# Kernel tuning notes

Measured on AMD Instinct MI355X. Metric: run time of the kernel, lower is better.

## Reference

```python
import jax, jax.numpy as jnp
import numpy as np

EPS = 1e-5  # torch BatchNorm default eps, eval mode with running stats

def _bn(x, g, b, m, v):
    shp = (1, -1) + (1,) * (x.ndim - 2)
    return (x - m.reshape(shp)) * (g.reshape(shp) / jnp.sqrt(v.reshape(shp) + EPS)) + b.reshape(shp)

def _lrelu(x):
    return jnp.where(x > 0, x, 0.2 * x)

def setup_inputs() -> dict:
    key = jax.random.key(0)
    ks = jax.random.split(key, 20)
    B, N, K = 4, 2048, 32
    Cin, Cf, Co = 6, 64, 64  # in_channels, feat_channels, out_channels(==nhiddens)
    f32 = jnp.float32
    def randn(k, shape, s=1.0):
        return jax.random.normal(k, shape, f32) * s
    def bnp(k, c):
        k1, k2, k3, k4 = jax.random.split(k, 4)
        return (randn(k1, (c,)), randn(k2, (c,)), randn(k3, (c,), 0.1),
                jax.random.uniform(k4, (c,), f32, 0.5, 1.5))
    inp = {
        "x": randn(ks[0], (B, Cin, N, K)),          # knn_points
        "y": randn(ks[1], (B, Cf, N, K)),           # knn_feat
        "points": randn(ks[2], (B, Cin // 2, N)),
        "feat": randn(ks[3], (B, Cf // 2, N)),
        "Wq": randn(ks[4], (Cf, Cf // 2), 0.1),
        "Wpos1": randn(ks[5], (Cin, Cin // 2), 0.1),
        "Wpos2": randn(ks[6], (Cf, Cin), 0.1),
        "Wattn": randn(ks[7], (Co * Cin, Cf), 0.1),
        "Wlin": randn(ks[8], (Co, Co), 0.1),
        "Wres": randn(ks[9], (Co, Cf), 0.1),
    }
    for name, k, c in [("q", ks[10], Cf), ("p", ks[11], Cin), ("a", ks[12], Co * Cin),
                       ("1", ks[13], Co), ("l", ks[14], Co), ("r", ks[15], Co)]:
        g, b, m, v = bnp(k, c)
        inp["g" + name], inp["b" + name], inp["m" + name], inp["v" + name] = g, b, m, v
    return inp

def reference(x, y, points, feat, Wq, Wpos1, Wpos2, Wattn, Wlin, Wres,
              gq, bq, mq, vq, gp, bp, mp, vp, ga, ba, ma, va,
              g1, b1, m1, v1, gl, bl, ml, vl, gr, br, mr, vr):
    B, Cin, N, K = x.shape
    Cf = y.shape[1]
    Co = Wattn.shape[0] // Cin
    # query projection (conv1d 1x1 == per-point GEMM) + BN + LeakyReLU
    x_q = _lrelu(_bn(jnp.einsum('oi,bin->bon', Wq, feat), gq, bq, mq, vq))   # [B,Cf,N]
    # positional branch
    pos = _lrelu(_bn(jnp.einsum('oi,bin->bon', Wpos1, points), gp, bp, mp, vp))  # [B,Cin,N]
    pos = pos[:, :, :, None] - x                                             # [B,Cin,N,K]
    pos = jnp.einsum('oi,bink->bonk', Wpos2, pos)                            # [B,Cf,N,K]
    # vector (subtraction) attention, softmax over neighbors k
    attn = x_q[:, :, :, None] - y + pos                                      # [B,Cf,N,K]
    attn = jax.nn.softmax(attn / float(np.sqrt(Cf)), axis=-1)
    attn = _bn(jnp.einsum('oi,bink->bonk', Wattn, attn), ga, ba, ma, va)     # [B,Co*Cin,N,K]
    # per-point tiny matmul: [Co,Cin] @ [Cin] for every (b,n,k)
    attn = attn.transpose(0, 2, 3, 1).reshape(B, N, K, Co, Cin)
    out = jnp.einsum('bnkoi,bnki->bonk', attn, x.transpose(0, 2, 3, 1))      # [B,Co,N,K]
    h = _lrelu(_bn(out, g1, b1, m1, v1))
    h = _bn(jnp.einsum('oi,bink->bonk', Wlin, h), gl, bl, ml, vl)
    res = _bn(jnp.einsum('oi,bink->bonk', Wres, y), gr, br, mr, vr)
    return _lrelu(h + res)
```

## Files before the change

kernel.cpp:

```cpp
#include <hip/hip_runtime.h>

constexpr int NB  = 4;
constexpr int NPT = 2048;
constexpr int KNN = 32;
constexpr int CIN = 6;
constexpr int CF  = 64;
constexpr int CO  = 64;
constexpr float EPS = 1e-5f;

typedef short bf16x8 __attribute__((ext_vector_type(8)));
typedef float f32x4  __attribute__((ext_vector_type(4)));

constexpr size_t WS_WA  = 0;
constexpr size_t WS_WL  = 49152;
constexpr size_t WS_WR  = 57344;
constexpr size_t WS_BA  = 65536;
constexpr size_t WS_BNF = 67072;

__device__ __host__ inline unsigned short bf16_rne(float f) {
  unsigned u = __builtin_bit_cast(unsigned, f);
  u += 0x7fffu + ((u >> 16) & 1u);
  return (unsigned short)(u >> 16);
}

__global__ void setup_kernel(const float *Wattn, const float *Wlin, const float *Wres,
                             const float *ga, const float *ba, const float *ma, const float *va,
                             const float *g1, const float *b1, const float *m1, const float *v1,
                             const float *gl, const float *bl, const float *ml, const float *vl,
                             const float *gr, const float *br, const float *mr, const float *vr,
                             unsigned short *WAf, unsigned short *WLf, unsigned short *WRf,
                             float *baP, float *bnf) {
  const int t = blockIdx.x * blockDim.x + threadIdx.x;
  const int stride = gridDim.x * blockDim.x;
  for (int e = t; e < 6 * 4 * 2 * 64 * 8; e += stride) {
    const int j = e & 7, l = (e >> 3) & 63, ks = (e >> 9) & 1, ot = (e >> 10) & 3, i = e >> 12;
    const int m = l & 15, cg = l >> 4;
    const int cc = ks * 32 + cg * 8 + j;
    const int row = (ot * 16 + m) * CIN + i;
    const float sa = ga[row] * rsqrtf(va[row] + EPS);
    WAf[e] = bf16_rne(Wattn[row * CF + cc] * sa);
  }
  for (int e = t; e < 4 * 2 * 64 * 8; e += stride) {
    const int j = e & 7, l = (e >> 3) & 63, ks = (e >> 9) & 1, ot = e >> 10;
    const int m = l & 15;
    const int cc = ks * 32 + (l >> 4) * 8 + j;
    const int row = ot * 16 + m;
    const float sl = gl[row] * rsqrtf(vl[row] + EPS);
    const float sr = gr[row] * rsqrtf(vr[row] + EPS);
    WLf[e] = bf16_rne(Wlin[row * CF + cc] * sl);
    WRf[e] = bf16_rne(Wres[row * CF + cc] * sr);
  }
  for (int e = t; e < 384; e += stride) {
    const int i = e >> 6, o = e & 63;
    const int j0 = o * CIN + i;
    const float sa = ga[j0] * rsqrtf(va[j0] + EPS);
    baP[e] = ba[j0] - ma[j0] * sa;
  }
  for (int e = t; e < 64; e += stride) {
    const float s1v = g1[e] * rsqrtf(v1[e] + EPS);
    bnf[e]      = s1v;
    bnf[64 + e] = b1[e] - m1[e] * s1v;
    const float slv = gl[e] * rsqrtf(vl[e] + EPS);
    const float srv = gr[e] * rsqrtf(vr[e] + EPS);
    bnf[128 + e] = (bl[e] - ml[e] * slv) + (br[e] - mr[e] * srv);
  }
}

struct Params {
  const float *x, *y, *points, *feat;
  const float *Wq, *Wpos1, *Wpos2;
  const float *gq, *bq, *mq, *vq;
  const float *gp, *bp, *mp, *vp;
  const unsigned short *WAf, *WLf, *WRf;
  const float *baP, *bnf;
  float *out;
};

__global__ __launch_bounds__(256) void fused_pt_attn(Params p) {
  const int tid  = threadIdx.x;
  const int lane = tid & 63;
  const int wid  = tid >> 6;
  const int bid  = ((blockIdx.x & 7) << 8) + (blockIdx.x >> 3);
  const int pidx = bid * 4 + wid;
  const int b    = pidx >> 11;
  const int n    = pidx & (NPT - 1);

  __shared__ unsigned short s_B[4][2048];
  __shared__ float s_d[4][192];
  __shared__ float s_f[4][32];
  unsigned short *BB = s_B[wid];
  float *dW = s_d[wid];
  float *fW = s_f[wid];

  float ftv = 0.f, ptv = 0.f;
  if (lane < 32) ftv = p.feat[((size_t)b * 32 + lane) * NPT + n];
  if (lane < 3)  ptv = p.points[((size_t)b * 3 + lane) * NPT + n];
  const int xi = lane >> 3, xk = (lane & 7) * 4;
  float4 x4 = make_float4(0.f, 0.f, 0.f, 0.f);
  if (lane < 48)
    x4 = *(const float4 *)(p.x + (((size_t)b * CIN + xi) * NPT + n) * KNN + xk);
  const float *w2p = p.Wpos2 + lane * 6;
  const float2 w2a = *(const float2 *)(w2p);
  const float2 w2b = *(const float2 *)(w2p + 2);
  const float2 w2c = *(const float2 *)(w2p + 4);
  const float w2[6] = {w2a.x, w2a.y, w2b.x, w2b.y, w2c.x, w2c.y};

  if (lane < 32) fW[lane] = ftv;

  const float pt0 = __shfl(ptv, 0), pt1 = __shfl(ptv, 1), pt2 = __shfl(ptv, 2);
  float pos1[6];
#pragma unroll
  for (int i = 0; i < 6; ++i) {
    const float a = p.Wpos1[i * 3 + 0] * pt0 + p.Wpos1[i * 3 + 1] * pt1 +
                    p.Wpos1[i * 3 + 2] * pt2;
    const float s = p.gp[i] * rsqrtf(p.vp[i] + EPS);
    const float v = fmaf(a, s, p.bp[i] - p.mp[i] * s);
    pos1[i] = v > 0.f ? v : 0.2f * v;
  }

  if (lane < 48) {
    float pi = pos1[0];
    pi = (xi == 1) ? pos1[1] : pi;
    pi = (xi == 2) ? pos1[2] : pi;
    pi = (xi == 3) ? pos1[3] : pi;
    pi = (xi == 4) ? pos1[4] : pi;
    pi = (xi == 5) ? pos1[5] : pi;
    *(float4 *)(dW + xi * 32 + xk) =
        make_float4(pi - x4.x, pi - x4.y, pi - x4.z, pi - x4.w);
  }

  float xq;
  {
    float acc = 0.f;
    const float *wq = p.Wq + lane * 32;
#pragma unroll
    for (int q = 0; q < 8; ++q) {
      const float4 w4 = *(const float4 *)(wq + q * 4);
      const float4 f4 = *(const float4 *)(fW + q * 4);
      acc = fmaf(w4.x, f4.x, fmaf(w4.y, f4.y, fmaf(w4.z, f4.z, fmaf(w4.w, f4.w, acc))));
    }
    const float s = p.gq[lane] * rsqrtf(p.vq[lane] + EPS);
    const float v = fmaf(acc, s, p.bq[lane] - p.mq[lane] * s);
    xq = v > 0.f ? v : 0.2f * v;
  }

  float pre[32];
#pragma unroll
  for (int k = 0; k < 32; ++k) pre[k] = 0.f;
#pragma unroll
  for (int i = 0; i < 6; ++i) {
    const float wv = w2[i];
#pragma unroll
    for (int q = 0; q < 8; ++q) {
      const float4 d4 = *(const float4 *)(dW + i * 32 + q * 4);
      pre[q * 4 + 0] = fmaf(wv, d4.x, pre[q * 4 + 0]);
      pre[q * 4 + 1] = fmaf(wv, d4.y, pre[q * 4 + 1]);
      pre[q * 4 + 2] = fmaf(wv, d4.z, pre[q * 4 + 2]);
      pre[q * 4 + 3] = fmaf(wv, d4.w, pre[q * 4 + 3]);
    }
  }

  const float *yrow = p.y + (((size_t)b * CF + lane) * NPT + n) * KNN;
#pragma unroll
  for (int q = 0; q < 8; ++q) {
    const float4 y4 = *(const float4 *)(yrow + q * 4);
    const float yv[4] = {y4.x, y4.y, y4.z, y4.w};
#pragma unroll
    for (int j = 0; j < 4; ++j) {
      const int k = q * 4 + j;
      BB[k * 64 + (lane ^ ((k & 7) << 3))] = bf16_rne(yv[j]);
      pre[k] = (xq - yv[j] + pre[k]) * 0.125f;
    }
  }

  const int og = lane >> 4, kl = lane & 15;
  const int swz = (kl & 7) << 3;

  bf16x8 By[2][2];
#pragma unroll
  for (int ks = 0; ks < 2; ++ks)
#pragma unroll
    for (int nt = 0; nt < 2; ++nt)
      By[ks][nt] = *(const bf16x8 *)(BB + (kl + nt * 16) * 64 +
                                     ((ks * 32 + og * 8) ^ swz));

  float mx = pre[0];
#pragma unroll
  for (int k = 1; k < 32; ++k) mx = fmaxf(mx, pre[k]);
  float sum = 0.f;
#pragma unroll
  for (int k = 0; k < 32; ++k) {
    pre[k] = __expf(pre[k] - mx);
    BB[k * 64 + (lane ^ ((k & 7) << 3))] = bf16_rne(pre[k]);
    sum += pre[k];
  }
  const float inv = 1.f / sum;

  float xvv[6][2];
#pragma unroll
  for (int i = 0; i < 6; ++i)
#pragma unroll
    for (int nt = 0; nt < 2; ++nt)
      xvv[i][nt] = pos1[i] - dW[i * 32 + kl + nt * 16];

  bf16x8 Ba[2][2];
#pragma unroll
  for (int ks = 0; ks < 2; ++ks)
#pragma unroll
    for (int nt = 0; nt < 2; ++nt)
      Ba[ks][nt] = *(const bf16x8 *)(BB + (kl + nt * 16) * 64 +
                                     ((ks * 32 + og * 8) ^ swz));

  const bf16x8 *WAv = (const bf16x8 *)p.WAf;
#pragma unroll
  for (int ot = 0; ot < 4; ++ot) {
    float out1[2][4] = {{0.f, 0.f, 0.f, 0.f}, {0.f, 0.f, 0.f, 0.f}};
#pragma unroll
    for (int i = 0; i < 6; ++i) {
      const bf16x8 A0 = WAv[((i * 4 + ot) * 2 + 0) * 64 + lane];
      const bf16x8 A1 = WAv[((i * 4 + ot) * 2 + 1) * 64 + lane];
      const f32x4 ba4 = *(const f32x4 *)(p.baP + i * 64 + ot * 16 + og * 4);
#pragma unroll
      for (int nt = 0; nt < 2; ++nt) {
        f32x4 g = {0.f, 0.f, 0.f, 0.f};
        g = __builtin_amdgcn_mfma_f32_16x16x32_bf16(A0, Ba[0][nt], g, 0, 0, 0);
        g = __builtin_amdgcn_mfma_f32_16x16x32_bf16(A1, Ba[1][nt], g, 0, 0, 0);
        const float xv = xvv[i][nt];
#pragma unroll
        for (int r = 0; r < 4; ++r)
          out1[nt][r] = fmaf(fmaf(g[r], inv, ba4[r]), xv, out1[nt][r]);
      }
    }
    const f32x4 s14 = *(const f32x4 *)(p.bnf + 0 * 64 + ot * 16 + og * 4);
    const f32x4 b14 = *(const f32x4 *)(p.bnf + 1 * 64 + ot * 16 + og * 4);
#pragma unroll
    for (int nt = 0; nt < 2; ++nt) {
      const int kcol = kl + nt * 16;
      unsigned hp[4];
#pragma unroll
      for (int r = 0; r < 4; ++r) {
        const float t = fmaf(s14[r], out1[nt][r], b14[r]);
        hp[r] = bf16_rne(t > 0.f ? t : 0.2f * t);
      }
      const int idx = kcol * 64 + ((ot * 16 + og * 4) ^ swz);
      *(uint2 *)(BB + idx) = make_uint2(hp[0] | (hp[1] << 16), hp[2] | (hp[3] << 16));
    }
  }

  bf16x8 Bh[2][2];
#pragma unroll
  for (int ks = 0; ks < 2; ++ks)
#pragma unroll
    for (int nt = 0; nt < 2; ++nt)
      Bh[ks][nt] = *(const bf16x8 *)(BB + (kl + nt * 16) * 64 +
                                     ((ks * 32 + og * 8) ^ swz));

  const bf16x8 *WLv = (const bf16x8 *)p.WLf;
  const bf16x8 *WRv = (const bf16x8 *)p.WRf;
#pragma unroll
  for (int ot = 0; ot < 4; ++ot) {
    const bf16x8 L0 = WLv[(ot * 2 + 0) * 64 + lane];
    const bf16x8 L1 = WLv[(ot * 2 + 1) * 64 + lane];
    const bf16x8 R0 = WRv[(ot * 2 + 0) * 64 + lane];
    const bf16x8 R1 = WRv[(ot * 2 + 1) * 64 + lane];
    const f32x4 blr = *(const f32x4 *)(p.bnf + 2 * 64 + ot * 16 + og * 4);
#pragma unroll
    for (int nt = 0; nt < 2; ++nt) {
      f32x4 a = {0.f, 0.f, 0.f, 0.f};
      a = __builtin_amdgcn_mfma_f32_16x16x32_bf16(L0, Bh[0][nt], a, 0, 0, 0);
      a = __builtin_amdgcn_mfma_f32_16x16x32_bf16(L1, Bh[1][nt], a, 0, 0, 0);
      a = __builtin_amdgcn_mfma_f32_16x16x32_bf16(R0, By[0][nt], a, 0, 0, 0);
      a = __builtin_amdgcn_mfma_f32_16x16x32_bf16(R1, By[1][nt], a, 0, 0, 0);
      const int kcol = kl + nt * 16;
      float *ob = p.out + (((size_t)(b * CO + ot * 16 + og * 4)) * NPT + n) * KNN + kcol;
#pragma unroll
      for (int r = 0; r < 4; ++r) {
        const float v = a[r] + blr[r];
        ob[(size_t)r * NPT * KNN] = v > 0.f ? v : 0.2f * v;
      }
    }
  }
}

extern "C" void kernel_launch(void *const *d_in, const int *in_sizes, int n_in,
                              void *d_out, int out_size, void *d_ws, size_t ws_size,
                              hipStream_t stream) {
  char *ws = (char *)d_ws;
  unsigned short *WAf = (unsigned short *)(ws + WS_WA);
  unsigned short *WLf = (unsigned short *)(ws + WS_WL);
  unsigned short *WRf = (unsigned short *)(ws + WS_WR);
  float *baP = (float *)(ws + WS_BA);
  float *bnf = (float *)(ws + WS_BNF);

  setup_kernel<<<dim3(96), dim3(256), 0, stream>>>(
      (const float *)d_in[7], (const float *)d_in[8], (const float *)d_in[9],
      (const float *)d_in[18], (const float *)d_in[19], (const float *)d_in[20], (const float *)d_in[21],
      (const float *)d_in[22], (const float *)d_in[23], (const float *)d_in[24], (const float *)d_in[25],
      (const float *)d_in[26], (const float *)d_in[27], (const float *)d_in[28], (const float *)d_in[29],
      (const float *)d_in[30], (const float *)d_in[31], (const float *)d_in[32], (const float *)d_in[33],
      WAf, WLf, WRf, baP, bnf);

  Params p;
  p.x      = (const float *)d_in[0];
  p.y      = (const float *)d_in[1];
  p.points = (const float *)d_in[2];
  p.feat   = (const float *)d_in[3];
  p.Wq     = (const float *)d_in[4];
  p.Wpos1  = (const float *)d_in[5];
  p.Wpos2  = (const float *)d_in[6];
  p.gq = (const float *)d_in[10]; p.bq = (const float *)d_in[11];
  p.mq = (const float *)d_in[12]; p.vq = (const float *)d_in[13];
  p.gp = (const float *)d_in[14]; p.bp = (const float *)d_in[15];
  p.mp = (const float *)d_in[16]; p.vp = (const float *)d_in[17];
  p.WAf = WAf; p.WLf = WLf; p.WRf = WRf;
  p.baP = baP; p.bnf = bnf;
  p.out = (float *)d_out;

  fused_pt_attn<<<dim3(NB * NPT / 4), dim3(256), 0, stream>>>(p);
}
```

Before: 70.16 us.

## Prefetch y early, use exp2 softmax, packed bf16 converts, split MFMA accumulators

```diff
diff --git a/kernel.cpp b/kernel.cpp
--- a/kernel.cpp
+++ b/kernel.cpp
@@ -1,4 +1,5 @@
 #include <hip/hip_runtime.h>
+#include <hip/hip_bf16.h>
 
 constexpr int NB  = 4;
 constexpr int NPT = 2048;
@@ -7,6 +8,7 @@
 constexpr int CF  = 64;
 constexpr int CO  = 64;
 constexpr float EPS = 1e-5f;
+constexpr float S2  = 0.125f * 1.44269504f;
 
 typedef short bf16x8 __attribute__((ext_vector_type(8)));
 typedef float f32x4  __attribute__((ext_vector_type(4)));
@@ -21,6 +23,13 @@
   unsigned u = __builtin_bit_cast(unsigned, f);
   u += 0x7fffu + ((u >> 16) & 1u);
   return (unsigned short)(u >> 16);
+}
+
+__device__ inline unsigned pk2(float a, float b) {
+  __hip_bfloat162 h = __float22bfloat162_rn(float2{a, b});
+  unsigned u;
+  __builtin_memcpy(&u, &h, 4);
+  return u;
 }
 
 __global__ void setup_kernel(const float *Wattn, const float *Wlin, const float *Wres,
@@ -92,6 +101,11 @@
   float *dW = s_d[wid];
   float *fW = s_f[wid];
 
+  const float *yrow = p.y + (((size_t)b * CF + lane) * NPT + n) * KNN;
+  float4 y4[8];
+#pragma unroll
+  for (int q = 0; q < 8; ++q) y4[q] = *(const float4 *)(yrow + q * 4);
+
   float ftv = 0.f, ptv = 0.f;
   if (lane < 32) ftv = p.feat[((size_t)b * 32 + lane) * NPT + n];
   if (lane < 3)  ptv = p.points[((size_t)b * 3 + lane) * NPT + n];
@@ -160,17 +174,23 @@
     }
   }
 
-  const float *yrow = p.y + (((size_t)b * CF + lane) * NPT + n) * KNN;
+  const float xqs = xq * S2;
+#pragma unroll
+  for (int k = 0; k < 32; ++k) pre[k] = fmaf(pre[k], S2, xqs);
+
 #pragma unroll
   for (int q = 0; q < 8; ++q) {
-    const float4 y4 = *(const float4 *)(yrow + q * 4);
-    const float yv[4] = {y4.x, y4.y, y4.z, y4.w};
-#pragma unroll
-    for (int j = 0; j < 4; ++j) {
-      const int k = q * 4 + j;
-      BB[k * 64 + (lane ^ ((k & 7) << 3))] = bf16_rne(yv[j]);
-      pre[k] = (xq - yv[j] + pre[k]) * 0.125f;
-    }
+    const int k0 = q * 4;
+    const unsigned w0 = pk2(y4[q].x, y4[q].y);
+    const unsigned w1 = pk2(y4[q].z, y4[q].w);
+    BB[(k0 + 0) * 64 + (lane ^ (((k0 + 0) & 7) << 3))] = (unsigned short)w0;
+    BB[(k0 + 1) * 64 + (lane ^ (((k0 + 1) & 7) << 3))] = (unsigned short)(w0 >> 16);
+    BB[(k0 + 2) * 64 + (lane ^ (((k0 + 2) & 7) << 3))] = (unsigned short)w1;
+    BB[(k0 + 3) * 64 + (lane ^ (((k0 + 3) & 7) << 3))] = (unsigned short)(w1 >> 16);
+    pre[k0 + 0] = fmaf(-S2, y4[q].x, pre[k0 + 0]);
+    pre[k0 + 1] = fmaf(-S2, y4[q].y, pre[k0 + 1]);
+    pre[k0 + 2] = fmaf(-S2, y4[q].z, pre[k0 + 2]);
+    pre[k0 + 3] = fmaf(-S2, y4[q].w, pre[k0 + 3]);
   }
 
   const int og = lane >> 4, kl = lane & 15;
@@ -184,24 +204,40 @@
       By[ks][nt] = *(const bf16x8 *)(BB + (kl + nt * 16) * 64 +
                                      ((ks * 32 + og * 8) ^ swz));
 
-  float mx = pre[0];
-#pragma unroll
-  for (int k = 1; k < 32; ++k) mx = fmaxf(mx, pre[k]);
-  float sum = 0.f;
-#pragma unroll
-  for (int k = 0; k < 32; ++k) {
-    pre[k] = __expf(pre[k] - mx);
-    BB[k * 64 + (lane ^ ((k & 7) << 3))] = bf16_rne(pre[k]);
-    sum += pre[k];
-  }
-  const float inv = 1.f / sum;
-
-  float xvv[6][2];
+  float mx0 = pre[0], mx1 = pre[1], mx2 = pre[2], mx3 = pre[3];
+#pragma unroll
+  for (int k = 4; k < 32; k += 4) {
+    mx0 = fmaxf(mx0, pre[k]);
+    mx1 = fmaxf(mx1, pre[k + 1]);
+    mx2 = fmaxf(mx2, pre[k + 2]);
+    mx3 = fmaxf(mx3, pre[k + 3]);
+  }
+  const float mx = fmaxf(fmaxf(mx0, mx1), fmaxf(mx2, mx3));
+  float s0 = 0.f, s1 = 0.f, s2 = 0.f, s3 = 0.f;
+#pragma unroll
+  for (int k = 0; k < 32; k += 4) {
+    const float e0 = exp2f(pre[k + 0] - mx);
+    const float e1 = exp2f(pre[k + 1] - mx);
+    const float e2 = exp2f(pre[k + 2] - mx);
+    const float e3 = exp2f(pre[k + 3] - mx);
+    s0 += e0; s1 += e1; s2 += e2; s3 += e3;
+    const unsigned w0 = pk2(e0, e1);
+    const unsigned w1 = pk2(e2, e3);
+    BB[(k + 0) * 64 + (lane ^ (((k + 0) & 7) << 3))] = (unsigned short)w0;
+    BB[(k + 1) * 64 + (lane ^ (((k + 1) & 7) << 3))] = (unsigned short)(w0 >> 16);
+    BB[(k + 2) * 64 + (lane ^ (((k + 2) & 7) << 3))] = (unsigned short)w1;
+    BB[(k + 3) * 64 + (lane ^ (((k + 3) & 7) << 3))] = (unsigned short)(w1 >> 16);
+  }
+  const float inv = __builtin_amdgcn_rcpf((s0 + s1) + (s2 + s3));
+
+  float xvv[6][2], ivx[6][2];
 #pragma unroll
   for (int i = 0; i < 6; ++i)
 #pragma unroll
-    for (int nt = 0; nt < 2; ++nt)
+    for (int nt = 0; nt < 2; ++nt) {
       xvv[i][nt] = pos1[i] - dW[i * 32 + kl + nt * 16];
+      ivx[i][nt] = inv * xvv[i][nt];
+    }
 
   bf16x8 Ba[2][2];
 #pragma unroll
@@ -214,36 +250,44 @@
   const bf16x8 *WAv = (const bf16x8 *)p.WAf;
 #pragma unroll
   for (int ot = 0; ot < 4; ++ot) {
-    float out1[2][4] = {{0.f, 0.f, 0.f, 0.f}, {0.f, 0.f, 0.f, 0.f}};
+    f32x4 o0 = {0.f, 0.f, 0.f, 0.f}, o1 = o0;
+#pragma unroll
+    for (int i = 0; i < 6; ++i) {
+      const f32x4 ba4 = *(const f32x4 *)(p.baP + i * 64 + ot * 16 + og * 4);
+#pragma unroll
+      for (int r = 0; r < 4; ++r) {
+        o0[r] = fmaf(ba4[r], xvv[i][0], o0[r]);
+        o1[r] = fmaf(ba4[r], xvv[i][1], o1[r]);
+      }
+    }
 #pragma unroll
     for (int i = 0; i < 6; ++i) {
       const bf16x8 A0 = WAv[((i * 4 + ot) * 2 + 0) * 64 + lane];
       const bf16x8 A1 = WAv[((i * 4 + ot) * 2 + 1) * 64 + lane];
-      const f32x4 ba4 = *(const f32x4 *)(p.baP + i * 64 + ot * 16 + og * 4);
-#pragma unroll
-      for (int nt = 0; nt < 2; ++nt) {
-        f32x4 g = {0.f, 0.f, 0.f, 0.f};
-        g = __builtin_amdgcn_mfma_f32_16x16x32_bf16(A0, Ba[0][nt], g, 0, 0, 0);
-        g = __builtin_amdgcn_mfma_f32_16x16x32_bf16(A1, Ba[1][nt], g, 0, 0, 0);
-        const float xv = xvv[i][nt];
-#pragma unroll
-        for (int r = 0; r < 4; ++r)
-          out1[nt][r] = fmaf(fmaf(g[r], inv, ba4[r]), xv, out1[nt][r]);
-      }
+      f32x4 g = {0.f, 0.f, 0.f, 0.f};
+      g = __builtin_amdgcn_mfma_f32_16x16x32_bf16(A0, Ba[0][0], g, 0, 0, 0);
+      g = __builtin_amdgcn_mfma_f32_16x16x32_bf16(A1, Ba[1][0], g, 0, 0, 0);
+#pragma unroll
+      for (int r = 0; r < 4; ++r) o0[r] = fmaf(g[r], ivx[i][0], o0[r]);
+      g = (f32x4){0.f, 0.f, 0.f, 0.f};
+      g = __builtin_amdgcn_mfma_f32_16x16x32_bf16(A0, Ba[0][1], g, 0, 0, 0);
+      g = __builtin_amdgcn_mfma_f32_16x16x32_bf16(A1, Ba[1][1], g, 0, 0, 0);
+#pragma unroll
+      for (int r = 0; r < 4; ++r) o1[r] = fmaf(g[r], ivx[i][1], o1[r]);
     }
     const f32x4 s14 = *(const f32x4 *)(p.bnf + 0 * 64 + ot * 16 + og * 4);
     const f32x4 b14 = *(const f32x4 *)(p.bnf + 1 * 64 + ot * 16 + og * 4);
 #pragma unroll
     for (int nt = 0; nt < 2; ++nt) {
-      const int kcol = kl + nt * 16;
-      unsigned hp[4];
+      const f32x4 &oo = nt ? o1 : o0;
+      float t[4];
 #pragma unroll
       for (int r = 0; r < 4; ++r) {
-        const float t = fmaf(s14[r], out1[nt][r], b14[r]);
-        hp[r] = bf16_rne(t > 0.f ? t : 0.2f * t);
+        const float v = fmaf(s14[r], oo[r], b14[r]);
+        t[r] = v > 0.f ? v : 0.2f * v;
       }
-      const int idx = kcol * 64 + ((ot * 16 + og * 4) ^ swz);
-      *(uint2 *)(BB + idx) = make_uint2(hp[0] | (hp[1] << 16), hp[2] | (hp[3] << 16));
+      const int idx = (kl + nt * 16) * 64 + ((ot * 16 + og * 4) ^ swz);
+      *(uint2 *)(BB + idx) = make_uint2(pk2(t[0], t[1]), pk2(t[2], t[3]));
     }
   }
 
@@ -266,16 +310,16 @@
     const f32x4 blr = *(const f32x4 *)(p.bnf + 2 * 64 + ot * 16 + og * 4);
 #pragma unroll
     for (int nt = 0; nt < 2; ++nt) {
-      f32x4 a = {0.f, 0.f, 0.f, 0.f};
-      a = __builtin_amdgcn_mfma_f32_16x16x32_bf16(L0, Bh[0][nt], a, 0, 0, 0);
-      a = __builtin_amdgcn_mfma_f32_16x16x32_bf16(L1, Bh[1][nt], a, 0, 0, 0);
-      a = __builtin_amdgcn_mfma_f32_16x16x32_bf16(R0, By[0][nt], a, 0, 0, 0);
-      a = __builtin_amdgcn_mfma_f32_16x16x32_bf16(R1, By[1][nt], a, 0, 0, 0);
+      f32x4 aL = {0.f, 0.f, 0.f, 0.f}, aR = aL;
+      aL = __builtin_amdgcn_mfma_f32_16x16x32_bf16(L0, Bh[0][nt], aL, 0, 0, 0);
+      aL = __builtin_amdgcn_mfma_f32_16x16x32_bf16(L1, Bh[1][nt], aL, 0, 0, 0);
+      aR = __builtin_amdgcn_mfma_f32_16x16x32_bf16(R0, By[0][nt], aR, 0, 0, 0);
+      aR = __builtin_amdgcn_mfma_f32_16x16x32_bf16(R1, By[1][nt], aR, 0, 0, 0);
       const int kcol = kl + nt * 16;
       float *ob = p.out + (((size_t)(b * CO + ot * 16 + og * 4)) * NPT + n) * KNN + kcol;
 #pragma unroll
       for (int r = 0; r < 4; ++r) {
-        const float v = a[r] + blr[r];
+        const float v = (aL[r] + aR[r]) + blr[r];
         ob[(size_t)r * NPT * KNN] = v > 0.f ? v : 0.2f * v;
       }
     }
@@ -310,8 +354,8 @@
   p.Wpos2  = (const float *)d_in[6];
   p.gq = (const float *)d_in[10]; p.bq = (const float *)d_in[11];
   p.mq = (const float *)d_in[12]; p.vq = (const float *)d_in[13];
+  p.mp = (const float *)d_in[16]; p.vp = (const float *)d_in[17];
   p.gp = (const float *)d_in[14]; p.bp = (const float *)d_in[15];
-  p.mp = (const float *)d_in[16]; p.vp = (const float *)d_in[17];
   p.WAf = WAf; p.WLf = WLf; p.WRf = WRf;
   p.baP = baP; p.bnf = bnf;
   p.out = (float *)d_out;
```

New measurement: 84.31 us. 1.2x slower.
